# Optimization experiments

Measured on AMD Instinct MI355X. Metric: run time of the kernel, lower is better.

The kernel has to match this reference:

```python
import jax, jax.numpy as jnp
import numpy as np

R = 2          # total_rel
N = 6144       # total_ent / num nodes
H1 = 256       # layer 1 out
H2 = 256       # layer 2 out


def setup_inputs() -> dict:
    key = jax.random.key(0)
    k_adj, k_w1, k_c1, k_w2, k_c2 = jax.random.split(key, 5)
    adj = jax.random.uniform(k_adj, (R, N, N), dtype=jnp.float32)
    bw1 = jax.random.normal(k_w1, (R, N, H1), dtype=jnp.float32) * (1.0 / np.sqrt(N))
    bc1 = jax.random.normal(k_c1, (R, R), dtype=jnp.float32)
    bw2 = jax.random.normal(k_w2, (R, H1, H2), dtype=jnp.float32) * (1.0 / np.sqrt(H1))
    bc2 = jax.random.normal(k_c2, (R, R), dtype=jnp.float32)
    return {"adj": adj, "bw1": bw1, "bc1": bc1, "bw2": bw2, "bc2": bc2}


def _layer_weights(coeff, basis):
    # (R, n_basis) x (n_basis, in, out) -> (R*in, out)
    w = jnp.einsum('ij,jmn->imn', coeff, basis)
    return w.reshape(w.shape[0] * w.shape[1], w.shape[2])


def reference(adj, bw1, bc1, bw2, bc2):
    # --- layer 1: node_init is None -> features are dense adjacencies ---
    w1 = _layer_weights(bc1, bw1)                        # (R*N, H1)
    # cat([adj[0], adj[1]], axis=1) == transpose+reshape  (N, R*N)
    tmp1 = adj.transpose(1, 0, 2).reshape(N, R * N)
    out1 = tmp1 @ w1                                     # (N, H1)

    # --- layer 2: relu then per-relation spmm + basis matmul ---
    x = jax.nn.relu(out1)
    w2 = _layer_weights(bc2, bw2)                        # (R*H1, H2)
    # cat([adj[r] @ x for r], axis=1) as one einsum       (N, R*H1)
    tmp2 = jnp.einsum('rij,jd->ird', adj, x).reshape(N, R * H1)
    out2 = tmp2 @ w2                                     # (N, H2)

    final_rep = jnp.concatenate([out1, out2], axis=1)    # (N, H1+H2)
    final_rep = jnp.sum(final_rep, axis=0).reshape(-1, H1 + H2)  # (1, H1+H2)
    return (out2, final_rep)
```

## Files before the change

### kernel.cpp

```cpp
#include <hip/hip_runtime.h>


#define NN 6144
#define HH 256
#define SPLIT 8
#define KCHUNK 1536
#define KSTEPS 24

typedef __attribute__((ext_vector_type(4))) float f32x4;
typedef __attribute__((ext_vector_type(8))) unsigned short u16x8;
typedef __attribute__((ext_vector_type(4))) unsigned short u16x4;

__device__ __forceinline__ unsigned short f2bf(float f) {
  unsigned int u = __float_as_uint(f);
  u += 0x7FFFu + ((u >> 16) & 1u);
  return (unsigned short)(u >> 16);
}
__device__ __forceinline__ float bf2f(unsigned short h) {
  return __uint_as_float(((unsigned int)h) << 16);
}

__device__ __forceinline__ void mfma_bf16(f32x4& d, u16x8 a, u16x8 b) {
  asm("v_mfma_f32_16x16x32_bf16 %0, %1, %2, %0" : "+v"(d) : "v"(a), "v"(b));
}

__device__ __forceinline__ void gll16(const unsigned short* g, unsigned short* l) {
  __builtin_amdgcn_global_load_lds(
      (const __attribute__((address_space(1))) unsigned int*)g,
      (__attribute__((address_space(3))) unsigned int*)l,
      16, 0, 0);
}

__global__ void wgen_kernel(const float* __restrict__ basis,
                            const float* __restrict__ bc,
                            unsigned short* __restrict__ outw,
                            int tilesPerR, int jdim)
{
  __shared__ unsigned short wt[64][265];
  const int t  = blockIdx.x;
  const int r  = t / tilesPerR;
  const int jt = t % tilesPerR;
  const float c0 = bc[r * 2 + 0];
  const float c1 = bc[r * 2 + 1];
  const int tid = threadIdx.x;
  const float* b0 = basis + (size_t)jt * 64 * HH;
  const float* b1 = basis + (size_t)jdim * HH + (size_t)jt * 64 * HH;
#pragma unroll
  for (int k = 0; k < 16; ++k) {
    int idx = tid + k * 256;
    int row = idx >> 6;
    int c4  = (idx & 63) * 4;
    f32x4 v0 = *(const f32x4*)(b0 + (size_t)row * HH + c4);
    f32x4 v1 = *(const f32x4*)(b1 + (size_t)row * HH + c4);
    wt[row][c4 + 0] = f2bf(c0 * v0.x + c1 * v1.x);
    wt[row][c4 + 1] = f2bf(c0 * v0.y + c1 * v1.y);
    wt[row][c4 + 2] = f2bf(c0 * v0.z + c1 * v1.z);
    wt[row][c4 + 3] = f2bf(c0 * v0.w + c1 * v1.w);
  }
  __syncthreads();
#pragma unroll
  for (int k = 0; k < 8; ++k) {
    int chunk = tid + k * 256;
    int h  = chunk >> 3;
    int sp = chunk & 7;
    int j0 = (sp ^ (h & 7)) * 8;
    u16x8 v;
#pragma unroll
    for (int e = 0; e < 8; ++e) v[e] = wt[j0 + e][h];
    *(u16x8*)(outw + ((size_t)t * 2048 + chunk) * 8) = v;
  }
}

__global__ __launch_bounds__(256, 2) void gemm_adj_kernel(
    const float* __restrict__ adj, const unsigned short* __restrict__ Bws,
    unsigned short* __restrict__ Pp)
{
  __shared__ __align__(16) unsigned short Alds[2][64 * 64];
  __shared__ __align__(16) unsigned short Blds[2][256 * 64];
  const int tid  = threadIdx.x;
  const int lane = tid & 63;
  const int wave = tid >> 6;
  const int mb = blockIdx.x;
  const int s  = blockIdx.y;
  const int i0 = mb * 64;
  const int kbase = s * KCHUNK;
  const int rrel  = kbase / NN;
  const int jb    = kbase % NN;
  const int tBase = kbase / 64;

  const int arow = tid >> 3;
  const int acol = (tid & 7) * 8;
  const float* aPtr = adj + (size_t)rrel * NN * NN
                      + (size_t)(i0 + arow) * NN + jb + acol;
  const unsigned short* bPtr = Bws + (size_t)tBase * 2048 * 8 + (size_t)tid * 8;

  f32x4 acc[4][4];
#pragma unroll
  for (int m = 0; m < 4; ++m)
#pragma unroll
    for (int n = 0; n < 4; ++n) acc[m][n] = (f32x4){0.f, 0.f, 0.f, 0.f};

  f32x4 av0[2][2], av1[2][2];

#define ISSUE_A(SET, KK) do {                                                  \
    _Pragma("unroll")                                                          \
    for (int it = 0; it < 2; ++it) {                                           \
      SET[it][0] = *(const f32x4*)(aPtr + (size_t)it * 32 * NN + (KK) * 64);   \
      SET[it][1] = *(const f32x4*)(aPtr + (size_t)it * 32 * NN + (KK) * 64 + 4);\
    } } while (0)

#define ISSUE_B(BUF, KK) do {                                                  \
    _Pragma("unroll")                                                          \
    for (int c = 0; c < 8; ++c)                                                \
      gll16(bPtr + (size_t)(KK) * 2048 * 8 + c * 256 * 8,                      \
            (unsigned short*)((char*)Blds[BUF] + ((size_t)c * 256 + tid) * 16)); \
    } while (0)

#define STAGE_A(SET, BUF) do {                                                 \
    _Pragma("unroll")                                                          \
    for (int it = 0; it < 2; ++it) {                                           \
      int row = arow + it * 32;                                                \
      u16x8 w;                                                                 \
      w[0] = f2bf(SET[it][0].x); w[1] = f2bf(SET[it][0].y);                    \
      w[2] = f2bf(SET[it][0].z); w[3] = f2bf(SET[it][0].w);                    \
      w[4] = f2bf(SET[it][1].x); w[5] = f2bf(SET[it][1].y);                    \
      w[6] = f2bf(SET[it][1].z); w[7] = f2bf(SET[it][1].w);                    \
      *(u16x8*)((char*)Alds[BUF] + row * 128 +                                 \
                ((((tid & 7) ^ (row & 7))) << 4)) = w;                         \
    } } while (0)

#define COMPUTE(BUF) do {                                                      \
    _Pragma("unroll")                                                          \
    for (int ks = 0; ks < 2; ++ks) {                                           \
      u16x8 af[4], bfr[4];                                                     \
      _Pragma("unroll")                                                        \
      for (int m = 0; m < 4; ++m) {                                            \
        int row = m * 16 + (lane & 15);                                        \
        int off = (ks * 64 + ((lane >> 4) << 4)) ^ ((row & 7) << 4);           \
        af[m] = *(const u16x8*)((const char*)Alds[BUF] + row * 128 + off);     \
      }                                                                        \
      _Pragma("unroll")                                                        \
      for (int n = 0; n < 4; ++n) {                                            \
        int row = wave * 64 + n * 16 + (lane & 15);                            \
        int off = (ks * 64 + ((lane >> 4) << 4)) ^ ((row & 7) << 4);           \
        bfr[n] = *(const u16x8*)((const char*)Blds[BUF] + row * 128 + off);    \
      }                                                                        \
      _Pragma("unroll")                                                        \
      for (int m = 0; m < 4; ++m)                                              \
        _Pragma("unroll")                                                      \
        for (int n = 0; n < 4; ++n)                                            \
          mfma_bf16(acc[m][n], af[m], bfr[n]);                                 \
    } } while (0)

  ISSUE_B(0, 0);
  ISSUE_A(av0, 0);
  ISSUE_A(av1, 1);
  STAGE_A(av0, 0);
  __syncthreads();

  for (int kk = 0; kk < KSTEPS; kk += 2) {
    ISSUE_B(1, kk + 1);
    if (kk + 2 < KSTEPS) ISSUE_A(av0, kk + 2);
    COMPUTE(0);
    STAGE_A(av1, 1);
    __syncthreads();
    if (kk + 2 < KSTEPS) {
      ISSUE_B(0, kk + 2);
      if (kk + 3 < KSTEPS) ISSUE_A(av1, kk + 3);
    }
    COMPUTE(1);
    if (kk + 2 < KSTEPS) STAGE_A(av0, 0);
    __syncthreads();
  }
#undef ISSUE_A
#undef ISSUE_B
#undef STAGE_A
#undef COMPUTE

  unsigned short* P = Pp + ((size_t)s * NN + i0) * HH;
#pragma unroll
  for (int m = 0; m < 4; ++m)
#pragma unroll
    for (int n = 0; n < 4; ++n) {
      int col = wave * 64 + n * 16 + (lane & 15);
#pragma unroll
      for (int q = 0; q < 4; ++q) {
        int row = m * 16 + ((lane >> 4) << 2) + q;
        P[(size_t)row * HH + col] = f2bf(acc[m][n][q]);
      }
    }
}

__global__ __launch_bounds__(256, 2) void gemm_y_kernel(
    const unsigned short* __restrict__ xws, const unsigned short* __restrict__ w2ws,
    unsigned short* __restrict__ B2ws)
{
  __shared__ __align__(16) unsigned short Alds[64 * 64];
  __shared__ __align__(16) unsigned short Blds[256 * 64];
  const int tid  = threadIdx.x;
  const int lane = tid & 63;
  const int wave = tid >> 6;
  const int mb = blockIdx.x;
  const int r  = blockIdx.y;

  f32x4 acc[4][4];
#pragma unroll
  for (int m = 0; m < 4; ++m)
#pragma unroll
    for (int n = 0; n < 4; ++n) acc[m][n] = (f32x4){0.f, 0.f, 0.f, 0.f};

  for (int dt = 0; dt < 4; ++dt) {
    u16x8 avv[2];
    avv[0] = *(const u16x8*)(xws + (((size_t)(mb * 4 + dt)) * 512 + tid) * 8);
    avv[1] = *(const u16x8*)(xws + (((size_t)(mb * 4 + dt)) * 512 + 256 + tid) * 8);
    u16x8 bv[8];
#pragma unroll
    for (int c = 0; c < 8; ++c)
      bv[c] = *(const u16x8*)(w2ws + (((size_t)(r * 4 + dt)) * 2048 + c * 256 + tid) * 8);
    __syncthreads();
    *(u16x8*)(Alds + (size_t)tid * 8) = avv[0];
    *(u16x8*)(Alds + ((size_t)256 + tid) * 8) = avv[1];
#pragma unroll
    for (int c = 0; c < 8; ++c)
      *(u16x8*)(Blds + ((size_t)c * 256 + tid) * 8) = bv[c];
    __syncthreads();
#pragma unroll
    for (int ks = 0; ks < 2; ++ks) {
      u16x8 af[4], bfr[4];
#pragma unroll
      for (int m = 0; m < 4; ++m) {
        int row = m * 16 + (lane & 15);
        int off = (ks * 64 + ((lane >> 4) << 4)) ^ ((row & 7) << 4);
        af[m] = *(const u16x8*)((const char*)Alds + row * 128 + off);
      }
#pragma unroll
      for (int n = 0; n < 4; ++n) {
        int row = wave * 64 + n * 16 + (lane & 15);
        int off = (ks * 64 + ((lane >> 4) << 4)) ^ ((row & 7) << 4);
        bfr[n] = *(const u16x8*)((const char*)Blds + row * 128 + off);
      }
#pragma unroll
      for (int m = 0; m < 4; ++m)
#pragma unroll
        for (int n = 0; n < 4; ++n)
          mfma_bf16(acc[m][n], af[m], bfr[n]);
    }
  }
  const int tg = r * 96 + mb;
#pragma unroll
  for (int m = 0; m < 4; ++m) {
    int scont = m * 2 + ((lane >> 4) >> 1);
    int e0    = ((lane >> 4) & 1) * 4;
#pragma unroll
    for (int n = 0; n < 4; ++n) {
      int h   = wave * 64 + n * 16 + (lane & 15);
      int pos = scont ^ (h & 7);
      u16x4 v;
      v[0] = f2bf(acc[m][n][0]); v[1] = f2bf(acc[m][n][1]);
      v[2] = f2bf(acc[m][n][2]); v[3] = f2bf(acc[m][n][3]);
      *(u16x4*)(B2ws + (((size_t)tg * 2048 + h * 8 + pos) * 8 + e0)) = v;
    }
  }
}

__global__ void reduce1_kernel(const unsigned short* __restrict__ Pp,
                               unsigned short* __restrict__ xws,
                               float* __restrict__ fin)
{
  __shared__ float csm[8][256];
  const int tid = threadIdx.x;
  const int b   = blockIdx.x;
  const int hc  = tid & 31;
  const int rg  = tid >> 5;
  const int dt    = hc >> 3;
  const int scont = hc & 7;
  float cs[8] = {0.f, 0.f, 0.f, 0.f, 0.f, 0.f, 0.f, 0.f};
  for (int k = 0; k < 8; ++k) {
    int i = b * 64 + rg + k * 8;
    float sv[8] = {0.f, 0.f, 0.f, 0.f, 0.f, 0.f, 0.f, 0.f};
#pragma unroll
    for (int s = 0; s < SPLIT; ++s) {
      u16x8 v = *(const u16x8*)(Pp + ((size_t)s * NN + i) * HH + hc * 8);
#pragma unroll
      for (int e = 0; e < 8; ++e) sv[e] += bf2f(v[e]);
    }
    u16x8 xv;
#pragma unroll
    for (int e = 0; e < 8; ++e) {
      cs[e] += sv[e];
      xv[e] = f2bf(fmaxf(sv[e], 0.f));
    }
    int pos = scont ^ (i & 7);
    *(u16x8*)(xws + (((size_t)(b * 4 + dt)) * 512 + (i & 63) * 8 + pos) * 8) = xv;
  }
#pragma unroll
  for (int e = 0; e < 8; ++e) csm[rg][hc * 8 + e] = cs[e];
  __syncthreads();
  float v = 0.f;
#pragma unroll
  for (int r8 = 0; r8 < 8; ++r8) v += csm[r8][tid];
  atomicAdd(&fin[tid], v);
}

__global__ void reduce2_kernel(const unsigned short* __restrict__ Pp,
                               float* __restrict__ outp,
                               float* __restrict__ fin)
{
  __shared__ float csm[8][256];
  const int tid = threadIdx.x;
  const int b   = blockIdx.x;
  const int hc  = tid & 31;
  const int rg  = tid >> 5;
  float cs[8] = {0.f, 0.f, 0.f, 0.f, 0.f, 0.f, 0.f, 0.f};
  for (int k = 0; k < 8; ++k) {
    int i = b * 64 + rg + k * 8;
    float sv[8] = {0.f, 0.f, 0.f, 0.f, 0.f, 0.f, 0.f, 0.f};
#pragma unroll
    for (int s = 0; s < SPLIT; ++s) {
      u16x8 v = *(const u16x8*)(Pp + ((size_t)s * NN + i) * HH + hc * 8);
#pragma unroll
      for (int e = 0; e < 8; ++e) sv[e] += bf2f(v[e]);
    }
    float* o = outp + (size_t)i * HH + hc * 8;
    *(f32x4*)o = (f32x4){sv[0], sv[1], sv[2], sv[3]};
    *(f32x4*)(o + 4) = (f32x4){sv[4], sv[5], sv[6], sv[7]};
#pragma unroll
    for (int e = 0; e < 8; ++e) cs[e] += sv[e];
  }
#pragma unroll
  for (int e = 0; e < 8; ++e) csm[rg][hc * 8 + e] = cs[e];
  __syncthreads();
  float v = 0.f;
#pragma unroll
  for (int r8 = 0; r8 < 8; ++r8) v += csm[r8][tid];
  atomicAdd(&fin[256 + tid], v);
}

__global__ void zero_fin_kernel(float* fin) {
  fin[blockIdx.x * 256 + threadIdx.x] = 0.f;
}

extern "C" void kernel_launch(void* const* d_in, const int* in_sizes, int n_in,
                              void* d_out, int out_size, void* d_ws, size_t ws_size,
                              hipStream_t stream)
{
  const float* adj = (const float*)d_in[0];
  const float* bw1 = (const float*)d_in[1];
  const float* bc1 = (const float*)d_in[2];
  const float* bw2 = (const float*)d_in[3];
  const float* bc2 = (const float*)d_in[4];
  float* out2 = (float*)d_out;
  float* fin  = (float*)d_out + (size_t)NN * HH;

  char* ws = (char*)d_ws;
  unsigned short* Pp   = (unsigned short*)(ws + 0);
  unsigned short* B1ws = (unsigned short*)(ws + 25165824);
  unsigned short* B2ws = (unsigned short*)(ws + 31457280);
  unsigned short* xws  = (unsigned short*)(ws + 37748736);
  unsigned short* w2ws = (unsigned short*)(ws + 40894464);

  zero_fin_kernel<<<2, 256, 0, stream>>>(fin);
  wgen_kernel<<<192, 256, 0, stream>>>(bw1, bc1, B1ws, 96, NN);
  gemm_adj_kernel<<<dim3(96, SPLIT), 256, 0, stream>>>(adj, B1ws, Pp);
  reduce1_kernel<<<96, 256, 0, stream>>>(Pp, xws, fin);
  wgen_kernel<<<8, 256, 0, stream>>>(bw2, bc2, w2ws, 4, HH);
  gemm_y_kernel<<<dim3(96, 2), 256, 0, stream>>>(xws, w2ws, B2ws);
  gemm_adj_kernel<<<dim3(96, SPLIT), 256, 0, stream>>>(adj, B2ws, Pp);
  reduce2_kernel<<<96, 256, 0, stream>>>(Pp, out2, fin);
}
```

Before: 228.0 us.

## Single-buffer LDS in adjacency GEMM for higher occupancy and merge prep kernels

```diff
diff --git a/kernel.cpp b/kernel.cpp
--- a/kernel.cpp
+++ b/kernel.cpp
@@ -24,25 +24,25 @@
   asm("v_mfma_f32_16x16x32_bf16 %0, %1, %2, %0" : "+v"(d) : "v"(a), "v"(b));
 }
 
-__device__ __forceinline__ void gll16(const unsigned short* g, unsigned short* l) {
-  __builtin_amdgcn_global_load_lds(
-      (const __attribute__((address_space(1))) unsigned int*)g,
-      (__attribute__((address_space(3))) unsigned int*)l,
-      16, 0, 0);
-}
-
-__global__ void wgen_kernel(const float* __restrict__ basis,
-                            const float* __restrict__ bc,
-                            unsigned short* __restrict__ outw,
-                            int tilesPerR, int jdim)
-{
+__global__ void prep_kernel(const float* __restrict__ bw1, const float* __restrict__ bc1,
+                            const float* __restrict__ bw2, const float* __restrict__ bc2,
+                            unsigned short* __restrict__ B1ws, unsigned short* __restrict__ w2ws,
+                            float* __restrict__ fin)
+{
+  const int b   = blockIdx.x;
+  const int tid = threadIdx.x;
+  if (b >= 200) { fin[(b - 200) * 256 + tid] = 0.f; return; }
+
+  const float* basis; const float* bc; unsigned short* outw;
+  int tilesPerR, jdim, t;
+  if (b < 192) { basis = bw1; bc = bc1; outw = B1ws; tilesPerR = 96; jdim = NN; t = b; }
+  else         { basis = bw2; bc = bc2; outw = w2ws; tilesPerR = 4;  jdim = HH; t = b - 192; }
+
   __shared__ unsigned short wt[64][265];
-  const int t  = blockIdx.x;
   const int r  = t / tilesPerR;
   const int jt = t % tilesPerR;
   const float c0 = bc[r * 2 + 0];
   const float c1 = bc[r * 2 + 1];
-  const int tid = threadIdx.x;
   const float* b0 = basis + (size_t)jt * 64 * HH;
   const float* b1 = basis + (size_t)jdim * HH + (size_t)jt * 64 * HH;
 #pragma unroll
@@ -71,12 +71,12 @@
   }
 }
 
-__global__ __launch_bounds__(256, 2) void gemm_adj_kernel(
+__global__ __launch_bounds__(256, 3) void gemm_adj_kernel(
     const float* __restrict__ adj, const unsigned short* __restrict__ Bws,
     unsigned short* __restrict__ Pp)
 {
-  __shared__ __align__(16) unsigned short Alds[2][64 * 64];
-  __shared__ __align__(16) unsigned short Blds[2][256 * 64];
+  __shared__ __align__(16) unsigned short Alds[64 * 64];
+  __shared__ __align__(16) unsigned short Blds[256 * 64];
   const int tid  = threadIdx.x;
   const int lane = tid & 63;
   const int wave = tid >> 6;
@@ -88,11 +88,9 @@
   const int jb    = kbase % NN;
   const int tBase = kbase / 64;
 
-  const int arow = tid >> 3;
-  const int acol = (tid & 7) * 8;
-  const float* aPtr = adj + (size_t)rrel * NN * NN
-                      + (size_t)(i0 + arow) * NN + jb + acol;
-  const unsigned short* bPtr = Bws + (size_t)tBase * 2048 * 8 + (size_t)tid * 8;
+  const float* aRow = adj + (size_t)rrel * NN * NN
+                      + (size_t)(i0 + (tid >> 4)) * NN + jb + (tid & 15) * 4;
+  const unsigned short* bBase = Bws + (size_t)tBase * 2048 * 8 + (size_t)tid * 8;
 
   f32x4 acc[4][4];
 #pragma unroll
@@ -100,36 +98,39 @@
 #pragma unroll
     for (int n = 0; n < 4; ++n) acc[m][n] = (f32x4){0.f, 0.f, 0.f, 0.f};
 
-  f32x4 av0[2][2], av1[2][2];
+  f32x4 av0[4], av1[4];
+  u16x8 bv[8];
 
 #define ISSUE_A(SET, KK) do {                                                  \
     _Pragma("unroll")                                                          \
-    for (int it = 0; it < 2; ++it) {                                           \
-      SET[it][0] = *(const f32x4*)(aPtr + (size_t)it * 32 * NN + (KK) * 64);   \
-      SET[it][1] = *(const f32x4*)(aPtr + (size_t)it * 32 * NN + (KK) * 64 + 4);\
+    for (int it = 0; it < 4; ++it)                                             \
+      SET[it] = *(const f32x4*)(aRow + (size_t)it * 16 * NN + (KK) * 64);      \
+  } while (0)
+
+#define ISSUE_B(KK) do {                                                       \
+    _Pragma("unroll")                                                          \
+    for (int c = 0; c < 8; ++c)                                                \
+      bv[c] = *(const u16x8*)(bBase + (size_t)(KK) * 2048 * 8 + c * 256 * 8);  \
+  } while (0)
+
+#define STAGE_A(SET) do {                                                      \
+    _Pragma("unroll")                                                          \
+    for (int it = 0; it < 4; ++it) {                                           \
+      int row = (tid >> 4) + it * 16;                                          \
+      int off = ((tid & 15) * 8) ^ ((row & 7) << 4);                           \
+      u16x4 w;                                                                 \
+      w[0] = f2bf(SET[it].x); w[1] = f2bf(SET[it].y);                          \
+      w[2] = f2bf(SET[it].z); w[3] = f2bf(SET[it].w);                          \
+      *(u16x4*)((char*)Alds + row * 128 + off) = w;                            \
     } } while (0)
 
-#define ISSUE_B(BUF, KK) do {                                                  \
+#define STAGE_B() do {                                                         \
     _Pragma("unroll")                                                          \
     for (int c = 0; c < 8; ++c)                                                \
-      gll16(bPtr + (size_t)(KK) * 2048 * 8 + c * 256 * 8,                      \
-            (unsigned short*)((char*)Blds[BUF] + ((size_t)c * 256 + tid) * 16)); \
-    } while (0)
-
-#define STAGE_A(SET, BUF) do {                                                 \
-    _Pragma("unroll")                                                          \
-    for (int it = 0; it < 2; ++it) {                                           \
-      int row = arow + it * 32;                                                \
-      u16x8 w;                                                                 \
-      w[0] = f2bf(SET[it][0].x); w[1] = f2bf(SET[it][0].y);                    \
-      w[2] = f2bf(SET[it][0].z); w[3] = f2bf(SET[it][0].w);                    \
-      w[4] = f2bf(SET[it][1].x); w[5] = f2bf(SET[it][1].y);                    \
-      w[6] = f2bf(SET[it][1].z); w[7] = f2bf(SET[it][1].w);                    \
-      *(u16x8*)((char*)Alds[BUF] + row * 128 +                                 \
-                ((((tid & 7) ^ (row & 7))) << 4)) = w;                         \
-    } } while (0)
-
-#define COMPUTE(BUF) do {                                                      \
+      *(u16x8*)(Blds + ((size_t)c * 256 + tid) * 8) = bv[c];                   \
+  } while (0)
+
+#define COMPUTE() do {                                                         \
     _Pragma("unroll")                                                          \
     for (int ks = 0; ks < 2; ++ks) {                                           \
       u16x8 af[4], bfr[4];                                                     \
@@ -137,13 +138,13 @@
       for (int m = 0; m < 4; ++m) {                                            \
         int row = m * 16 + (lane & 15);                                        \
         int off = (ks * 64 + ((lane >> 4) << 4)) ^ ((row & 7) << 4);           \
-        af[m] = *(const u16x8*)((const char*)Alds[BUF] + row * 128 + off);     \
+        af[m] = *(const u16x8*)((const char*)Alds + row * 128 + off);          \
       }                                                                        \
       _Pragma("unroll")                                                        \
       for (int n = 0; n < 4; ++n) {                                            \
         int row = wave * 64 + n * 16 + (lane & 15);                            \
         int off = (ks * 64 + ((lane >> 4) << 4)) ^ ((row & 7) << 4);           \
-        bfr[n] = *(const u16x8*)((const char*)Blds[BUF] + row * 128 + off);    \
+        bfr[n] = *(const u16x8*)((const char*)Blds + row * 128 + off);         \
       }                                                                        \
       _Pragma("unroll")                                                        \
       for (int m = 0; m < 4; ++m)                                              \
@@ -152,29 +153,30 @@
           mfma_bf16(acc[m][n], af[m], bfr[n]);                                 \
     } } while (0)
 
-  ISSUE_B(0, 0);
   ISSUE_A(av0, 0);
+  ISSUE_B(0);
   ISSUE_A(av1, 1);
-  STAGE_A(av0, 0);
-  __syncthreads();
 
   for (int kk = 0; kk < KSTEPS; kk += 2) {
-    ISSUE_B(1, kk + 1);
+    __syncthreads();
+    STAGE_A(av0);
+    STAGE_B();
+    __syncthreads();
+    ISSUE_B(kk + 1);
     if (kk + 2 < KSTEPS) ISSUE_A(av0, kk + 2);
-    COMPUTE(0);
-    STAGE_A(av1, 1);
-    __syncthreads();
-    if (kk + 2 < KSTEPS) {
-      ISSUE_B(0, kk + 2);
-      if (kk + 3 < KSTEPS) ISSUE_A(av1, kk + 3);
-    }
-    COMPUTE(1);
-    if (kk + 2 < KSTEPS) STAGE_A(av0, 0);
-    __syncthreads();
+    COMPUTE();
+    __syncthreads();
+    STAGE_A(av1);
+    STAGE_B();
+    __syncthreads();
+    if (kk + 2 < KSTEPS) ISSUE_B(kk + 2);
+    if (kk + 3 < KSTEPS) ISSUE_A(av1, kk + 3);
+    COMPUTE();
   }
 #undef ISSUE_A
 #undef ISSUE_B
 #undef STAGE_A
+#undef STAGE_B
 #undef COMPUTE
 
   unsigned short* P = Pp + ((size_t)s * NN + i0) * HH;
@@ -336,10 +338,6 @@
   atomicAdd(&fin[256 + tid], v);
 }
 
-__global__ void zero_fin_kernel(float* fin) {
-  fin[blockIdx.x * 256 + threadIdx.x] = 0.f;
-}
-
 extern "C" void kernel_launch(void* const* d_in, const int* in_sizes, int n_in,
                               void* d_out, int out_size, void* d_ws, size_t ws_size,
                               hipStream_t stream)
@@ -359,11 +357,9 @@
   unsigned short* xws  = (unsigned short*)(ws + 37748736);
   unsigned short* w2ws = (unsigned short*)(ws + 40894464);
 
-  zero_fin_kernel<<<2, 256, 0, stream>>>(fin);
-  wgen_kernel<<<192, 256, 0, stream>>>(bw1, bc1, B1ws, 96, NN);
+  prep_kernel<<<202, 256, 0, stream>>>(bw1, bc1, bw2, bc2, B1ws, w2ws, fin);
   gemm_adj_kernel<<<dim3(96, SPLIT), 256, 0, stream>>>(adj, B1ws, Pp);
   reduce1_kernel<<<96, 256, 0, stream>>>(Pp, xws, fin);
-  wgen_kernel<<<8, 256, 0, stream>>>(bw2, bc2, w2ws, 4, HH);
   gemm_y_kernel<<<dim3(96, 2), 256, 0, stream>>>(xws, w2ws, B2ws);
   gemm_adj_kernel<<<dim3(96, SPLIT), 256, 0, stream>>>(adj, B2ws, Pp);
   reduce2_kernel<<<96, 256, 0, stream>>>(Pp, out2, fin);
```

Result: faster. 197.2 us (-13.5%).
